# Kernel tuning notes

Measured on AMD Instinct MI355X. Metric: run time of the kernel, lower is better.

The kernel has to match this reference:

```python
import jax, jax.numpy as jnp
import numpy as np

N, T, I, H = 256, 256, 512, 512

def setup_inputs() -> dict:
    key = jax.random.key(0)
    ks = jax.random.split(key, 9)
    s = 1.0 / np.sqrt(H)  # torch GRUCell init scale
    x = jax.random.normal(ks[0], (N, T, I), jnp.float32)
    is_init = jax.random.bernoulli(ks[1], 0.05, (N, T))  # bool resets
    hx = jax.random.normal(ks[2], (N, T, H), jnp.float32)
    W_ih = jax.random.uniform(ks[3], (3 * H, I), jnp.float32, -s, s)
    W_hh = jax.random.uniform(ks[4], (3 * H, H), jnp.float32, -s, s)
    b_ih = jax.random.uniform(ks[5], (3 * H,), jnp.float32, -s, s)
    b_hh = jax.random.uniform(ks[6], (3 * H,), jnp.float32, -s, s)
    W_out = jax.random.uniform(ks[7], (H, H), jnp.float32, -s, s)
    b_out = jax.random.uniform(ks[8], (H,), jnp.float32, -s, s)
    return {"x": x, "hx": hx, "W_ih": W_ih, "W_hh": W_hh, "b_ih": b_ih,
            "b_hh": b_hh, "W_out": W_out, "b_out": b_out, "is_init": is_init}

def _gru_forward(x, hx, W_ih, W_hh, b_ih, b_hh, W_out, b_out, is_init):
    # recurrent_mode branch; learnable_init=False -> reset to zeros
    mask = is_init[..., None]                         # [N,T,1] bool
    h0 = jnp.where(mask[:, 0], 0.0, hx[:, 0])        # [N,H]
    # precompute input-to-hidden gates for all steps: [N,T,3H]
    xi = jnp.einsum('nti,gi->ntg', x, W_ih) + b_ih

    def step(h, inp):
        xi_t, m_t = inp                              # [N,3H], [N,1]
        h = jnp.where(m_t, 0.0, h)                   # per-step init masking
        hh = h @ W_hh.T + b_hh                       # [N,3H]
        xr, xz, xn = jnp.split(xi_t, 3, axis=-1)
        hr, hz, hn = jnp.split(hh, 3, axis=-1)
        r = jax.nn.sigmoid(xr + hr)
        z = jax.nn.sigmoid(xz + hz)
        n = jnp.tanh(xn + r * hn)
        h_new = (1.0 - z) * n + z * h
        return h_new, h_new

    hT, hs = jax.lax.scan(step, h0,
                          (xi.transpose(1, 0, 2), mask.transpose(1, 0, 2)))
    hs = hs.transpose(1, 0, 2)                       # [N,T,H]
    output = hs @ W_out.T + b_out                    # LazyLinear projection
    hx_out = jnp.broadcast_to(hT[:, None, :], (hT.shape[0], T, hT.shape[1]))
    return output, hx_out

def reference(x, hx, W_ih, W_hh, b_ih, b_hh, W_out, b_out, is_init):
    return _gru_forward(x, hx, W_ih, W_hh, b_ih, b_hh, W_out, b_out, is_init)
```

## Files before the change

### kernel.cpp

```cpp
#include <hip/hip_runtime.h>

#define NB 256
#define TT 256
#define II 512
#define HH 512
#define GG 1536

typedef unsigned short ushort_t;
typedef unsigned int uint_t;
typedef unsigned long long ull_t;
typedef __attribute__((ext_vector_type(8))) short short8;
typedef __attribute__((ext_vector_type(4))) float f32x4;

typedef __attribute__((address_space(3))) void lds_void;
typedef const __attribute__((address_space(1))) void glb_void;

__device__ __forceinline__ ushort_t f2bf(float f) {
  union { float f; unsigned int u; } x; x.f = f;
  unsigned int r = x.u + 0x7FFFu + ((x.u >> 16) & 1u);
  return (ushort_t)(r >> 16);
}
__device__ __forceinline__ float bf2f(ushort_t b) {
  union { unsigned int u; float f; } x; x.u = ((unsigned int)b) << 16;
  return x.f;
}
__device__ __forceinline__ float sigmoidf_(float x) {
  return __fdividef(1.0f, 1.0f + __expf(-x));
}
__device__ __forceinline__ float tanhf_(float x) {
  float t = __expf(2.0f * x);
  return 1.0f - __fdividef(2.0f, t + 1.0f);
}
__device__ __forceinline__ short8 pack8(float4 a, float4 b) {
  short8 r;
  r[0] = (short)f2bf(a.x); r[1] = (short)f2bf(a.y);
  r[2] = (short)f2bf(a.z); r[3] = (short)f2bf(a.w);
  r[4] = (short)f2bf(b.x); r[5] = (short)f2bf(b.y);
  r[6] = (short)f2bf(b.z); r[7] = (short)f2bf(b.w);
  return r;
}

__global__ void mask_detect_kernel(const unsigned char* __restrict__ src,
                                   unsigned char* __restrict__ mask8) {
  __shared__ int fByte, fOdd;
  const int tid = threadIdx.x;
  if (tid == 0) { fByte = 0; fOdd = 0; }
  __syncthreads();
  const uint_t* w = (const uint_t*)src;
  int ab = 0, ao = 0;
  for (int i = tid; i < NB * TT; i += blockDim.x) {
    if ((i & 3) == 1 && src[i]) ab = 1;
    if (i < 16384 && (i & 1) == 1 && w[i]) ao = 1;
  }
  if (ab) fByte = 1;
  if (ao) fOdd = 1;
  __syncthreads();
  const int isByte = fByte, isW32 = fOdd;
  for (int i = tid; i < NB * TT; i += blockDim.x) {
    unsigned char m;
    if (isByte)      m = src[i] ? 1 : 0;
    else if (isW32)  m = w[i] ? 1 : 0;
    else             m = w[2 * i] ? 1 : 0;
    mask8[i] = m;
  }
}

__global__ void cvt_f2bf(const float* __restrict__ src, ushort_t* __restrict__ dst,
                         int n4) {
  int stride = gridDim.x * blockDim.x;
  for (int i = blockIdx.x * blockDim.x + threadIdx.x; i < n4; i += stride) {
    const float4 v = reinterpret_cast<const float4*>(src)[i];
    ushort4 o;
    o.x = f2bf(v.x); o.y = f2bf(v.y); o.z = f2bf(v.z); o.w = f2bf(v.w);
    reinterpret_cast<ushort4*>(dst)[i] = o;
  }
}

__global__ void pack_whh(const float* __restrict__ W, ushort_t* __restrict__ out) {
  int idx = blockIdx.x * blockDim.x + threadIdx.x;
  if (idx >= 96 * 16 * 64) return;
  int l = idx & 63;
  int tk = idx >> 6;
  int tile = tk >> 4, kk = tk & 15;
  int row = tile * 16 + (l & 15);
  int k = kk * 32 + (l >> 4) * 8;
  const float* s = W + (size_t)row * HH + k;
  short8 v;
#pragma unroll
  for (int e = 0; e < 8; ++e) v[e] = (short)f2bf(s[e]);
  *reinterpret_cast<short8*>(out + (size_t)idx * 8) = v;
}

template <int AF32, int CF32>
__global__ __launch_bounds__(256) void gemm_bt(
    const void* __restrict__ Av, const ushort_t* __restrict__ B,
    const float* __restrict__ bias, void* __restrict__ Cv, int NC) {
  __shared__ ushort_t As[128 * 32];
  __shared__ ushort_t Bs[128 * 32];
  const int tid = threadIdx.x;
  const int lane = tid & 63;
  const int w = tid >> 6;
  const int wr = w >> 1, wc = w & 1;
  const int c15 = lane & 15, l4 = lane >> 4;
  const int mbase = blockIdx.x * 128;
  const int nbase = blockIdx.y * 128;

  const int rs = tid >> 2;
  const int kb = (tid & 3) * 8;

  f32x4 acc[4][4] = {};

  const float4* Bg = reinterpret_cast<const float4*>(B);
  auto bIdx = [&](int c, int kt) {
    return ((size_t)(nbase + rs + 64 * c) * 512 + kt * 32 + kb) >> 3;
  };
  float4 rb0 = Bg[bIdx(0, 0)], rb1 = Bg[bIdx(1, 0)];

  const float4* Agf = reinterpret_cast<const float4*>(Av);
  auto aEl = [&](int c, int kt) {
    return (size_t)(mbase + rs + 64 * c) * 512 + kt * 32 + kb;
  };
  float4 a0a, a0b, a1a, a1b;
  float4 h0, h1;
  if constexpr (AF32) {
    a0a = Agf[aEl(0, 0) >> 2]; a0b = Agf[(aEl(0, 0) >> 2) + 1];
    a1a = Agf[aEl(1, 0) >> 2]; a1b = Agf[(aEl(1, 0) >> 2) + 1];
  } else {
    h0 = Agf[aEl(0, 0) >> 3];
    h1 = Agf[aEl(1, 0) >> 3];
  }

  for (int kt = 0; kt < 16; ++kt) {
    __syncthreads();
    if constexpr (AF32) {
      *reinterpret_cast<short8*>(&As[(size_t)tid * 8]) = pack8(a0a, a0b);
      *reinterpret_cast<short8*>(&As[(size_t)(tid + 256) * 8]) = pack8(a1a, a1b);
    } else {
      reinterpret_cast<float4*>(As)[tid] = h0;
      reinterpret_cast<float4*>(As)[tid + 256] = h1;
    }
    reinterpret_cast<float4*>(Bs)[tid] = rb0;
    reinterpret_cast<float4*>(Bs)[tid + 256] = rb1;
    if (kt < 15) {
      if constexpr (AF32) {
        a0a = Agf[aEl(0, kt + 1) >> 2]; a0b = Agf[(aEl(0, kt + 1) >> 2) + 1];
        a1a = Agf[aEl(1, kt + 1) >> 2]; a1b = Agf[(aEl(1, kt + 1) >> 2) + 1];
      } else {
        h0 = Agf[aEl(0, kt + 1) >> 3];
        h1 = Agf[aEl(1, kt + 1) >> 3];
      }
      rb0 = Bg[bIdx(0, kt + 1)]; rb1 = Bg[bIdx(1, kt + 1)];
    }
    __syncthreads();
    short8 af[4], bq[4];
#pragma unroll
    for (int m = 0; m < 4; ++m)
      af[m] = *reinterpret_cast<const short8*>(&As[(wr * 64 + m * 16 + c15) * 32 + l4 * 8]);
#pragma unroll
    for (int n = 0; n < 4; ++n)
      bq[n] = *reinterpret_cast<const short8*>(&Bs[(wc * 64 + n * 16 + c15) * 32 + l4 * 8]);
#pragma unroll
    for (int m = 0; m < 4; ++m)
#pragma unroll
      for (int n = 0; n < 4; ++n)
        acc[m][n] = __builtin_amdgcn_mfma_f32_16x16x32_bf16(af[m], bq[n], acc[m][n], 0, 0, 0);
  }

#pragma unroll
  for (int n = 0; n < 4; ++n) {
    const int col = nbase + wc * 64 + n * 16 + c15;
    const float bv = bias[col];
#pragma unroll
    for (int m = 0; m < 4; ++m) {
      const int row = mbase + wr * 64 + m * 16 + l4 * 4;
#pragma unroll
      for (int q = 0; q < 4; ++q) {
        const float v = acc[m][n][q] + bv;
        if constexpr (CF32)
          reinterpret_cast<float*>(Cv)[(size_t)(row + q) * NC + col] = v;
        else
          reinterpret_cast<ushort_t*>(Cv)[(size_t)(row + q) * NC + col] = f2bf(v);
      }
    }
  }
}

__global__ __launch_bounds__(256, 1) void gru_rec(
    const ushort_t* __restrict__ xi, const ushort_t* __restrict__ Wpk,
    const float* __restrict__ hx, const float* __restrict__ bhh,
    const unsigned char* __restrict__ mask8,
    ushort_t* __restrict__ hs, float* __restrict__ hT,
    char* __restrict__ xch, uint_t* __restrict__ flags) {
  extern __shared__ ushort_t smem[];
  const int HAF_U = 65536, XIL_U = 73728, HST_U = 79872;

  const int tid = threadIdx.x;
  const int lane = tid & 63;
  const int w = tid >> 6;
  const int c15 = lane & 15, l4 = lane >> 4;
  const int bid = blockIdx.x;
  const int a = bid & 7;
  const int b = bid >> 3;
  const int n0 = b * 16;

  const int jl = w * 16 + c15;
  const int jfull = a * 64 + jl;
  const float br = bhh[jfull], bz = bhh[512 + jfull], bn = bhh[1024 + jfull];

#pragma unroll
  for (int g = 0; g < 2; ++g)
#pragma unroll
    for (int kk = 0; kk < 16; ++kk)
      __builtin_amdgcn_global_load_lds(
          (glb_void*)(Wpk + ((size_t)((g * 32 + a * 4 + w) * 16 + kk)) * 512 + lane * 8),
          (lds_void*)(smem + w * 16384 + (g * 16 + kk) * 512 + lane * 8), 16, 0, 0);

  const int wb2 = ((2 * 32 + a * 4 + w) * 16) * 512 + lane * 8;
  short8 wn[16];
#pragma unroll
  for (int kk = 0; kk < 16; ++kk)
    wn[kk] = *(const short8*)(Wpk + wb2 + kk * 512);

  size_t xg0, xg1 = 0;
  {
    int c = tid, s = c / 24, r = c % 24, g = r >> 3, p = r & 7;
    xg0 = ((size_t)(n0 + s) * TT) * GG + g * 512 + a * 64 + p * 8;
    if (tid < 128) {
      c = tid + 256; s = c / 24; r = c % 24; g = r >> 3; p = r & 7;
      xg1 = ((size_t)(n0 + s) * TT) * GG + g * 512 + a * 64 + p * 8;
    }
  }
  const int xl0 = tid * 8, xl1 = (tid + 256) * 8;

  char* slot0 = xch + (size_t)(b * 2) * 16384;
  char* slot1 = xch + (size_t)(b * 2 + 1) * 16384;

  const int ps = tid >> 4, pj = tid & 15;
  const int pOff = (2 * a + (pj >> 3)) * 1024 +
                   (ps + 16 * ((pj >> 1) & 3)) * 16 + (pj & 1) * 8;
  const int pSrc = HST_U + ps * 72 + pj * 4;

  float h[4];
#pragma unroll
  for (int q = 0; q < 4; ++q) {
    const int s = l4 * 4 + q;
    const bool mk0 = mask8[(size_t)(n0 + s) * TT] != 0;
    const float v = mk0 ? 0.0f : hx[((size_t)(n0 + s) * TT) * HH + jfull];
    h[q] = v;
    smem[HST_U + s * 72 + jl] = f2bf(v);
  }
  __syncthreads();
  {
    const ull_t v = *(const ull_t*)(smem + pSrc);
    __hip_atomic_store((ull_t*)(slot0 + pOff), v,
                       __ATOMIC_RELAXED, __HIP_MEMORY_SCOPE_AGENT);
  }
  __syncthreads();
  if (tid == 0)
    __hip_atomic_store(&flags[bid * 32], 1u, __ATOMIC_RELAXED,
                       __HIP_MEMORY_SCOPE_AGENT);

  for (int t = 0; t < TT; ++t) {
    ushort_t* xb = smem + XIL_U + (t & 1) * 3072;
    __builtin_amdgcn_global_load_lds((glb_void*)(xi + xg0 + (size_t)t * GG),
                                     (lds_void*)(xb + xl0), 16, 0, 0);
    if (tid < 128)
      __builtin_amdgcn_global_load_lds((glb_void*)(xi + xg1 + (size_t)t * GG),
                                       (lds_void*)(xb + xl1), 16, 0, 0);

    if (tid < 8) {
      const uint_t tgt = (uint_t)(t + 1);
      while (__hip_atomic_load(&flags[(b * 8 + tid) * 32], __ATOMIC_RELAXED,
                               __HIP_MEMORY_SCOPE_AGENT) < tgt) {}
    }
    __syncthreads();

    const char* src = (t & 1) ? slot1 : slot0;
#pragma unroll
    for (int i = 0; i < 8; ++i) {
      const int c = tid + i * 256;
      const ull_t v = __hip_atomic_load((const ull_t*)(src + c * 8),
                                        __ATOMIC_RELAXED,
                                        __HIP_MEMORY_SCOPE_AGENT);
      *(ull_t*)((char*)smem + HAF_U * 2 + c * 8) = v;
    }

    const bool domask = (t + 1 < TT);
    const int tn = domask ? (t + 1) : t;
    unsigned char mkv[4];
#pragma unroll
    for (int q = 0; q < 4; ++q)
      mkv[q] = mask8[(size_t)(n0 + l4 * 4 + q) * TT + tn];

    __syncthreads();

    short8 af[16];
#pragma unroll
    for (int kk = 0; kk < 16; ++kk)
      af[kk] = *(const short8*)((char*)smem + HAF_U * 2 + kk * 1024 + lane * 16);

    f32x4 a0 = {0.f, 0.f, 0.f, 0.f}, a1 = a0, a2 = a0;
#pragma unroll
    for (int kk = 0; kk < 16; ++kk) {
      const short8 w0 = *(const short8*)(smem + w * 16384 + kk * 512 + lane * 8);
      const short8 w1 = *(const short8*)(smem + w * 16384 + (16 + kk) * 512 + lane * 8);
      a0 = __builtin_amdgcn_mfma_f32_16x16x32_bf16(af[kk], w0, a0, 0, 0, 0);
      a1 = __builtin_amdgcn_mfma_f32_16x16x32_bf16(af[kk], w1, a1, 0, 0, 0);
      a2 = __builtin_amdgcn_mfma_f32_16x16x32_bf16(af[kk], wn[kk], a2, 0, 0, 0);
    }

#pragma unroll
    for (int q = 0; q < 4; ++q) {
      const int s = l4 * 4 + q;
      const float xr = bf2f(xb[s * 192 + jl]);
      const float xz = bf2f(xb[s * 192 + 64 + jl]);
      const float xn = bf2f(xb[s * 192 + 128 + jl]);
      const float rr = sigmoidf_(xr + a0[q] + br);
      const float zz = sigmoidf_(xz + a1[q] + bz);
      const float nn = tanhf_(xn + rr * (a2[q] + bn));
      const float hnew = (1.0f - zz) * nn + zz * h[q];
      __builtin_nontemporal_store(
          f2bf(hnew), &hs[((size_t)(n0 + s) * TT + t) * HH + jfull]);
      const float hp = (domask && mkv[q]) ? 0.0f : hnew;
      h[q] = hp;
      smem[HST_U + s * 72 + jl] = f2bf(hp);
    }
    __syncthreads();

    if (domask) {
      char* dst = ((t + 1) & 1) ? slot1 : slot0;
      const ull_t v = *(const ull_t*)(smem + pSrc);
      __hip_atomic_store((ull_t*)(dst + pOff), v,
                         __ATOMIC_RELAXED, __HIP_MEMORY_SCOPE_AGENT);
      __syncthreads();
      if (tid == 0)
        __hip_atomic_store(&flags[bid * 32], (uint_t)(t + 2), __ATOMIC_RELAXED,
                           __HIP_MEMORY_SCOPE_AGENT);
    }
  }

#pragma unroll
  for (int q = 0; q < 4; ++q)
    hT[(size_t)(n0 + l4 * 4 + q) * HH + jfull] = h[q];
}

__global__ void bcast_hT(const float* __restrict__ hT, float* __restrict__ dst) {
  const float4* s = (const float4*)hT;
  float4* d = (float4*)dst;
  const int total = NB * TT * HH / 4;
  const int stride = gridDim.x * blockDim.x;
  for (int c = blockIdx.x * blockDim.x + threadIdx.x; c < total; c += stride) {
    int n = c >> 15;
    int j4 = c & 127;
    d[c] = s[(n << 7) | j4];
  }
}

extern "C" void kernel_launch(void* const* d_in, const int* in_sizes, int n_in,
                              void* d_out, int out_size, void* d_ws, size_t ws_size,
                              hipStream_t stream) {
  const float* x    = (const float*)d_in[0];
  const float* hx   = (const float*)d_in[1];
  const float* Wih  = (const float*)d_in[2];
  const float* Whh  = (const float*)d_in[3];
  const float* bih  = (const float*)d_in[4];
  const float* bhh  = (const float*)d_in[5];
  const float* Wout = (const float*)d_in[6];
  const float* bout = (const float*)d_in[7];
  const unsigned char* isinit = (const unsigned char*)d_in[8];

  char* ws = (char*)d_ws;
  ushort_t* xi    = (ushort_t*)(ws);
  ushort_t* wihb  = (ushort_t*)(ws + 201326592);
  ushort_t* whhp  = (ushort_t*)(ws + 202899456);
  ushort_t* woutb = (ushort_t*)(ws + 204472320);
  unsigned char* mask8 = (unsigned char*)(ws + 204996608);
  float*    hTbuf = (float*)(ws + 205062144);
  uint_t*   flags = (uint_t*)(ws + 205586432);
  char*     xch   = (char*)(ws + 205602816);

  float* out1 = (float*)d_out;
  float* out2 = out1 + (size_t)NB * TT * HH;
  ushort_t* hsb = (ushort_t*)out2;

  hipMemsetAsync(flags, 0, 128 * 32 * sizeof(uint_t), stream);
  mask_detect_kernel<<<1, 1024, 0, stream>>>(isinit, mask8);
  cvt_f2bf<<<768, 256, 0, stream>>>(Wih, wihb, GG * II / 4);
  cvt_f2bf<<<256, 256, 0, stream>>>(Wout, woutb, HH * HH / 4);
  pack_whh<<<384, 256, 0, stream>>>(Whh, whhp);

  dim3 g1(512, 12);
  gemm_bt<1, 0><<<g1, 256, 0, stream>>>((const void*)x, wihb, bih, (void*)xi, GG);

  gru_rec<<<128, 256, 162048, stream>>>(xi, whhp, hx, bhh, mask8, hsb, hTbuf,
                                        xch, flags);

  dim3 g3(512, 4);
  gemm_bt<0, 1><<<g3, 256, 0, stream>>>((const void*)hsb, woutb, bout, (void*)out1, HH);

  bcast_hT<<<2048, 256, 0, stream>>>(hTbuf, out2);
}
```

Measured before the change: 1.669 ms.

## Replace flag-based cross-block sync with tagged hidden-state exchange words

Removes the separate per-block flag counters and the extra barriers around them. Each published bf16 hidden value now carries a 16-bit step tag in the same 32-bit word, and consumers spin on the data loads until every tag matches the expected step. The exchange buffer doubles in size and polling now covers all 16 words per thread, not 8 flag reads. The goal is to cut the flag round-trip and barriers off the serial recurrence critical path.

```diff
diff --git a/kernel.cpp b/kernel.cpp
--- a/kernel.cpp
+++ b/kernel.cpp
@@ -190,7 +190,7 @@
     const float* __restrict__ hx, const float* __restrict__ bhh,
     const unsigned char* __restrict__ mask8,
     ushort_t* __restrict__ hs, float* __restrict__ hT,
-    char* __restrict__ xch, uint_t* __restrict__ flags) {
+    char* __restrict__ xch) {
   extern __shared__ ushort_t smem[];
   const int HAF_U = 65536, XIL_U = 73728, HST_U = 79872;
 
@@ -232,13 +232,23 @@
   }
   const int xl0 = tid * 8, xl1 = (tid + 256) * 8;
 
-  char* slot0 = xch + (size_t)(b * 2) * 16384;
-  char* slot1 = xch + (size_t)(b * 2 + 1) * 16384;
+  char* slot0 = xch + (size_t)(b * 2) * 32768;
+  char* slot1 = xch + (size_t)(b * 2 + 1) * 32768;
 
   const int ps = tid >> 4, pj = tid & 15;
   const int pOff = (2 * a + (pj >> 3)) * 1024 +
                    (ps + 16 * ((pj >> 1) & 3)) * 16 + (pj & 1) * 8;
   const int pSrc = HST_U + ps * 72 + pj * 4;
+
+  auto publish = [&](char* slot, uint_t tag) {
+    const uint_t h0 = smem[pSrc], h1 = smem[pSrc + 1];
+    const uint_t h2 = smem[pSrc + 2], h3 = smem[pSrc + 3];
+    const ull_t w0 = ((ull_t)(h0 << 16 | tag)) | (((ull_t)(h1 << 16 | tag)) << 32);
+    const ull_t w1 = ((ull_t)(h2 << 16 | tag)) | (((ull_t)(h3 << 16 | tag)) << 32);
+    char* d = slot + (size_t)pOff * 2;
+    __hip_atomic_store((ull_t*)d, w0, __ATOMIC_RELAXED, __HIP_MEMORY_SCOPE_AGENT);
+    __hip_atomic_store((ull_t*)(d + 8), w1, __ATOMIC_RELAXED, __HIP_MEMORY_SCOPE_AGENT);
+  };
 
   float h[4];
 #pragma unroll
@@ -250,15 +260,7 @@
     smem[HST_U + s * 72 + jl] = f2bf(v);
   }
   __syncthreads();
-  {
-    const ull_t v = *(const ull_t*)(smem + pSrc);
-    __hip_atomic_store((ull_t*)(slot0 + pOff), v,
-                       __ATOMIC_RELAXED, __HIP_MEMORY_SCOPE_AGENT);
-  }
-  __syncthreads();
-  if (tid == 0)
-    __hip_atomic_store(&flags[bid * 32], 1u, __ATOMIC_RELAXED,
-                       __HIP_MEMORY_SCOPE_AGENT);
+  publish(slot0, 1u);
 
   for (int t = 0; t < TT; ++t) {
     ushort_t* xb = smem + XIL_U + (t & 1) * 3072;
@@ -268,21 +270,27 @@
       __builtin_amdgcn_global_load_lds((glb_void*)(xi + xg1 + (size_t)t * GG),
                                        (lds_void*)(xb + xl1), 16, 0, 0);
 
-    if (tid < 8) {
-      const uint_t tgt = (uint_t)(t + 1);
-      while (__hip_atomic_load(&flags[(b * 8 + tid) * 32], __ATOMIC_RELAXED,
-                               __HIP_MEMORY_SCOPE_AGENT) < tgt) {}
-    }
-    __syncthreads();
-
     const char* src = (t & 1) ? slot1 : slot0;
-#pragma unroll
-    for (int i = 0; i < 8; ++i) {
-      const int c = tid + i * 256;
-      const ull_t v = __hip_atomic_load((const ull_t*)(src + c * 8),
-                                        __ATOMIC_RELAXED,
-                                        __HIP_MEMORY_SCOPE_AGENT);
-      *(ull_t*)((char*)smem + HAF_U * 2 + c * 8) = v;
+    const uint_t tgt = (uint_t)(t + 1);
+    ull_t v[16];
+    bool ok;
+    do {
+      ok = true;
+#pragma unroll
+      for (int i = 0; i < 16; ++i)
+        v[i] = __hip_atomic_load((const ull_t*)(src + ((size_t)(tid + i * 256)) * 8),
+                                 __ATOMIC_RELAXED, __HIP_MEMORY_SCOPE_AGENT);
+#pragma unroll
+      for (int i = 0; i < 16; ++i)
+        ok &= (((uint_t)v[i] & 0xFFFFu) == tgt) &&
+              (((uint_t)(v[i] >> 32) & 0xFFFFu) == tgt);
+    } while (!ok);
+#pragma unroll
+    for (int i = 0; i < 16; ++i) {
+      const uint_t lo = (uint_t)(v[i] >> 16) & 0xFFFFu;
+      const uint_t hi = (uint_t)(v[i] >> 48);
+      *(uint_t*)((char*)smem + HAF_U * 2 + ((size_t)(tid + i * 256)) * 4) =
+          lo | (hi << 16);
     }
 
     const bool domask = (t + 1 < TT);
@@ -327,16 +335,8 @@
     }
     __syncthreads();
 
-    if (domask) {
-      char* dst = ((t + 1) & 1) ? slot1 : slot0;
-      const ull_t v = *(const ull_t*)(smem + pSrc);
-      __hip_atomic_store((ull_t*)(dst + pOff), v,
-                         __ATOMIC_RELAXED, __HIP_MEMORY_SCOPE_AGENT);
-      __syncthreads();
-      if (tid == 0)
-        __hip_atomic_store(&flags[bid * 32], (uint_t)(t + 2), __ATOMIC_RELAXED,
-                           __HIP_MEMORY_SCOPE_AGENT);
-    }
+    if (domask)
+      publish(((t + 1) & 1) ? slot1 : slot0, (uint_t)(t + 2));
   }
 
 #pragma unroll
@@ -376,14 +376,13 @@
   ushort_t* woutb = (ushort_t*)(ws + 204472320);
   unsigned char* mask8 = (unsigned char*)(ws + 204996608);
   float*    hTbuf = (float*)(ws + 205062144);
-  uint_t*   flags = (uint_t*)(ws + 205586432);
   char*     xch   = (char*)(ws + 205602816);
 
   float* out1 = (float*)d_out;
   float* out2 = out1 + (size_t)NB * TT * HH;
   ushort_t* hsb = (ushort_t*)out2;
 
-  hipMemsetAsync(flags, 0, 128 * 32 * sizeof(uint_t), stream);
+  hipMemsetAsync(xch, 0, 1 << 20, stream);
   mask_detect_kernel<<<1, 1024, 0, stream>>>(isinit, mask8);
   cvt_f2bf<<<768, 256, 0, stream>>>(Wih, wihb, GG * II / 4);
   cvt_f2bf<<<256, 256, 0, stream>>>(Wout, woutb, HH * HH / 4);
@@ -393,7 +392,7 @@
   gemm_bt<1, 0><<<g1, 256, 0, stream>>>((const void*)x, wihb, bih, (void*)xi, GG);
 
   gru_rec<<<128, 256, 162048, stream>>>(xi, whhp, hx, bhh, mask8, hsb, hTbuf,
-                                        xch, flags);
+                                        xch);
 
   dim3 g3(512, 4);
   gemm_bt<0, 1><<<g3, 256, 0, stream>>>((const void*)hsb, woutb, bout, (void*)out1, HH);
```

New measurement: 1.349 ms. 1.24x faster.
